# Kernel optimization log

Hardware: AMD Instinct MI355X
Metric: run time of the kernel (lower is better)

Reference implementation:

```python
import jax, jax.numpy as jnp
import numpy as np

SUB = 40   # subframe_size
NSUB = 4   # nb_subframes


def _glu(x, w):
    return x * jax.nn.sigmoid(x @ w.T)


def _gru(x, h, w_ih, w_hh):
    # torch.nn.GRUCell (bias=False): gates ordered r, z, n
    H = h.shape[-1]
    gi = x @ w_ih.T
    gh = h @ w_hh.T
    r = jax.nn.sigmoid(gi[:, :H] + gh[:, :H])
    z = jax.nn.sigmoid(gi[:, H:2 * H] + gh[:, H:2 * H])
    n = jnp.tanh(gi[:, 2 * H:] + r * gh[:, 2 * H:])
    return (1.0 - z) * n + z * h


def _fargan_forward(features, period, p):
    B, T, _ = features.shape
    period = jnp.clip(period, 32, 254)

    # ---- FARGANCond ----
    f = features[:, 2:, :]                               # [B, T-2, 20]
    pidx = jnp.clip(period[:, 2:] - 32, 0, 223)
    pe = p['pembed'][pidx]                               # [B, T-2, 12]
    x = jnp.tanh(jnp.concatenate([f, pe], -1) @ p['fd1_w'].T)   # [B, T-2, 64]
    y = jax.lax.conv_general_dilated(
        x.transpose(0, 2, 1), p['fconv1_w'], (1,), 'VALID',
        dimension_numbers=('NCH', 'OIH', 'NCH'))
    y = jnp.tanh(y).transpose(0, 2, 1)                   # [B, T-4, 128]
    cond = jnp.tanh(y @ p['fd2_w'].T)                    # [B, T-4, 320]

    nb_frames = T - 4
    cond_steps = cond.reshape(B, nb_frames, NSUB, 80)
    cond_steps = cond_steps.transpose(1, 2, 0, 3).reshape(nb_frames * NSUB, B, 80)
    pitch = period[:, 3:3 + nb_frames]                   # conv-center aligned pitch
    pitch_steps = jnp.repeat(pitch.T, NSUB, axis=0)      # [steps, B]

    rng = jnp.arange(SUB + 4)

    def step(carry, inp):
        exc_mem, prev_pred, s1, s2, s3, fwc_state = carry
        cond80, per = inp
        gain = 0.2 + 0.8 * jax.nn.sigmoid(cond80 @ p['cg_w'].T + p['cg_b'])
        gain = jnp.clip(gain, 0.001, 20.0)               # [B, 1]
        idx = 256 - per[:, None] + rng[None, :] - 2
        idx = idx - (idx >= 256) * per[:, None]
        idx = jnp.clip(idx, 0, 255)
        pred = jnp.take_along_axis(exc_mem, idx, axis=1) / (1e-5 + gain)  # [B, 44]
        prev = exc_mem[:, -SUB:] / (1e-5 + gain)         # [B, 40]
        tmp = jnp.concatenate([cond80, pred, prev], 1)   # [B, 164]
        fpitch = pred[:, 2:-2]                           # [B, 40]
        xcat = jnp.concatenate([fwc_state, tmp], 1)      # [B, 328]
        fwc_out = _glu(jnp.tanh(xcat @ p['fwc_w'].T), p['fwc_glu_w'])  # [B, 192]
        new_fwc_state = xcat[:, 164:]
        pg = jax.nn.sigmoid(fwc_out @ p['gout_w'].T + p['gout_b'])     # [B, 4]
        s1n = _gru(jnp.concatenate([fwc_out, pg[:, 0:1] * fpitch, prev], 1), s1, p['g1_ih'], p['g1_hh'])
        g1 = _glu(s1n, p['glu1_w'])
        s2n = _gru(jnp.concatenate([g1, pg[:, 1:2] * fpitch, prev], 1), s2, p['g2_ih'], p['g2_hh'])
        g2 = _glu(s2n, p['glu2_w'])
        s3n = _gru(jnp.concatenate([g2, pg[:, 2:3] * fpitch, prev], 1), s3, p['g3_ih'], p['g3_hh'])
        g3 = _glu(s3n, p['glu3_w'])
        skip_in = jnp.concatenate([g1, g2, g3, fwc_out, pg[:, 3:4] * fpitch, prev], 1)  # [B, 688+80]
        skip = _glu(jnp.tanh(skip_in @ p['skip_w'].T), p['skip_glu_w'])
        sig = jnp.tanh(skip @ p['sig_w'].T) * gain       # [B, 40]
        exc_mem = jnp.concatenate([exc_mem[:, SUB:], sig], 1)
        prev_pred = jnp.concatenate([prev_pred[:, SUB:], fpitch], 1)
        return (exc_mem, prev_pred, s1n, s2n, s3n, new_fwc_state), sig

    dt = features.dtype
    carry0 = (jnp.zeros((B, 256), dt), jnp.zeros((B, 256), dt),
              jnp.zeros((B, 160), dt), jnp.zeros((B, 128), dt),
              jnp.zeros((B, 128), dt), jnp.zeros((B, 164), dt))
    _, sigs = jax.lax.scan(jax.checkpoint(step), carry0, (cond_steps, pitch_steps))
    return sigs.transpose(1, 0, 2).reshape(B, -1)        # [B, nb_frames*160]


def _w(key, out_dim, in_dim):
    return jax.random.normal(key, (out_dim, in_dim), jnp.float32) / np.sqrt(in_dim)


def setup_inputs() -> dict:
    key = jax.random.key(0)
    ks = jax.random.split(key, 24)
    B, T = 128, 504
    d = {}
    d['features'] = jax.random.normal(ks[0], (B, T, 20), jnp.float32)
    d['period'] = jax.random.randint(ks[1], (B, T), 32, 255)
    d['pembed'] = jax.random.normal(ks[2], (224, 12), jnp.float32) * 0.3
    d['fd1_w'] = _w(ks[3], 64, 32)
    d['fconv1_w'] = jax.random.normal(ks[4], (128, 64, 3), jnp.float32) / np.sqrt(192.0)
    d['fd2_w'] = _w(ks[5], 320, 128)
    d['cg_w'] = _w(ks[6], 1, 80)
    d['cg_b'] = jnp.zeros((1,), jnp.float32)
    d['fwc_w'] = _w(ks[7], 192, 328)
    d['fwc_glu_w'] = _w(ks[8], 192, 192)
    d['g1_ih'] = _w(ks[9], 480, 272)
    d['g1_hh'] = _w(ks[10], 480, 160)
    d['glu1_w'] = _w(ks[11], 160, 160)
    d['g2_ih'] = _w(ks[12], 384, 240)
    d['g2_hh'] = _w(ks[13], 384, 128)
    d['glu2_w'] = _w(ks[14], 128, 128)
    d['g3_ih'] = _w(ks[15], 384, 208)
    d['g3_hh'] = _w(ks[16], 384, 128)
    d['glu3_w'] = _w(ks[17], 128, 128)
    d['skip_w'] = _w(ks[18], 128, 688)
    d['skip_glu_w'] = _w(ks[19], 128, 128)
    d['sig_w'] = _w(ks[20], 40, 128)
    d['gout_w'] = _w(ks[21], 4, 192)
    d['gout_b'] = jnp.zeros((4,), jnp.float32)
    return d


def reference(features, period, pembed, fd1_w, fconv1_w, fd2_w, cg_w, cg_b,
              fwc_w, fwc_glu_w, g1_ih, g1_hh, glu1_w, g2_ih, g2_hh, glu2_w,
              g3_ih, g3_hh, glu3_w, skip_w, skip_glu_w, sig_w, gout_w, gout_b):
    p = dict(pembed=pembed, fd1_w=fd1_w, fconv1_w=fconv1_w, fd2_w=fd2_w,
             cg_w=cg_w, cg_b=cg_b, fwc_w=fwc_w, fwc_glu_w=fwc_glu_w,
             g1_ih=g1_ih, g1_hh=g1_hh, glu1_w=glu1_w,
             g2_ih=g2_ih, g2_hh=g2_hh, glu2_w=glu2_w,
             g3_ih=g3_ih, g3_hh=g3_hh, glu3_w=glu3_w,
             skip_w=skip_w, skip_glu_w=skip_glu_w, sig_w=sig_w,
             gout_w=gout_w, gout_b=gout_b)
    return _fargan_forward(features, period, p)
```

## Files before the change

kernel.cpp:

```cpp
#include <hip/hip_runtime.h>
#include <hip/hip_fp16.h>
#include <math.h>


#define DEV __device__ __forceinline__

DEV float sigm(float x) { return 1.0f / (1.0f + __expf(-x)); }
DEV float tanh_f(float x) { return 1.0f - 2.0f / (__expf(2.0f * x) + 1.0f); }

typedef _Float16 h2v __attribute__((ext_vector_type(2)));

#if defined(__has_builtin)
#if __has_builtin(__builtin_amdgcn_fdot2)
#define HAVE_FDOT2 1
#endif
#endif

DEV float fdot2(h2v a, h2v b, float c) {
#ifdef HAVE_FDOT2
    return __builtin_amdgcn_fdot2(a, b, c, false);
#else
    return c + (float)a[0] * (float)b[0] + (float)a[1] * (float)b[1];
#endif
}

constexpr size_t STEPS = 2000;
constexpr size_t OFF_X     = 0;
constexpr size_t OFF_Y     = 4200000;
constexpr size_t OFF_GAIN  = 12392000;
constexpr size_t OFF_CONDH = 12648000;
constexpr size_t OFF_W     = 22888000;

constexpr size_t W_FWC     = 0;
constexpr size_t W_FWCGLU  = W_FWC    + 192*352;
constexpr size_t W_GOUT    = W_FWCGLU + 192*192;
constexpr size_t W_G1IH    = W_GOUT   + 4*192;
constexpr size_t W_G1HH    = W_G1IH   + 480*272;
constexpr size_t W_GLU1    = W_G1HH   + 480*160;
constexpr size_t W_G2IH    = W_GLU1   + 160*160;
constexpr size_t W_G2HH    = W_G2IH   + 384*240;
constexpr size_t W_GLU2    = W_G2HH   + 384*128;
constexpr size_t W_G3IH    = W_GLU2   + 128*128;
constexpr size_t W_G3HH    = W_G3IH   + 384*208;
constexpr size_t W_GLU3    = W_G3HH   + 384*128;
constexpr size_t W_SKIP    = W_GLU3   + 128*128;
constexpr size_t W_SKIPGLU = W_SKIP   + 128*704;
constexpr size_t W_SIG     = W_SKIPGLU+ 128*128;

__global__ void k_pack_h(const float* __restrict__ src, __half* __restrict__ dst,
                         int OUT, int K, int KP8) {
    int t = blockIdx.x * 256 + threadIdx.x;
    if (t >= OUT * KP8) return;
    int j = t % OUT;
    int k8 = t / OUT;
    __half* d = dst + (size_t)t * 8;
#pragma unroll
    for (int i = 0; i < 8; ++i) {
        int k = k8 * 8 + i;
        d[i] = (k < K) ? __float2half(src[(size_t)j * K + k]) : __float2half(0.0f);
    }
}

__global__ void k_feat(const float* __restrict__ features, const int* __restrict__ period,
                       const float* __restrict__ pembed, const float* __restrict__ fd1,
                       float* __restrict__ xbuf) {
    int t = blockIdx.x * 256 + threadIdx.x;
    const int total = 128 * 502 * 64;
    if (t >= total) return;
    int o = t & 63;
    int r = t >> 6;
    int ft = r % 502;
    int b = r / 502;
    const float* f = features + ((size_t)b * 504 + ft + 2) * 20;
    int per = period[b * 504 + ft + 2];
    per = min(max(per, 32), 254);
    const float* pe = pembed + (per - 32) * 12;
    const float* w = fd1 + o * 32;
    float acc = 0.0f;
#pragma unroll
    for (int i = 0; i < 20; ++i) acc += f[i] * w[i];
#pragma unroll
    for (int i = 0; i < 12; ++i) acc += pe[i] * w[20 + i];
    xbuf[t] = tanh_f(acc);
}

__global__ void k_conv(const float* __restrict__ xbuf, const float* __restrict__ fconv1,
                       float* __restrict__ ybuf) {
    int t = blockIdx.x * 256 + threadIdx.x;
    const int total = 128 * 500 * 128;
    if (t >= total) return;
    int oc = t & 127;
    int r = t >> 7;
    int tt = r % 500;
    int b = r / 500;
    const float* xp = xbuf + ((size_t)b * 502 + tt) * 64;
    const float* w = fconv1 + oc * 192;
    float acc = 0.0f;
#pragma unroll 8
    for (int i = 0; i < 64; ++i) {
        acc += xp[i] * w[i * 3 + 0];
        acc += xp[64 + i] * w[i * 3 + 1];
        acc += xp[128 + i] * w[i * 3 + 2];
    }
    ybuf[t] = tanh_f(acc);
}

__global__ void k_cond(const float* __restrict__ ybuf, const float* __restrict__ fd2,
                       __half* __restrict__ cond) {
    int b = blockIdx.x / 50;
    int t0 = (blockIdx.x % 50) * 10;
    int tid = threadIdx.x;
    __shared__ float yl[1280];
    for (int i = tid; i < 1280; i += 320)
        yl[i] = ybuf[((size_t)b * 500 + t0) * 128 + i];
    __syncthreads();
    const float* w = fd2 + tid * 128;
    float acc[10];
#pragma unroll
    for (int q = 0; q < 10; ++q) acc[q] = 0.0f;
#pragma unroll 4
    for (int k = 0; k < 128; ++k) {
        float wv = w[k];
#pragma unroll
        for (int q = 0; q < 10; ++q) acc[q] += wv * yl[q * 128 + k];
    }
#pragma unroll
    for (int q = 0; q < 10; ++q)
        cond[((size_t)b * 500 + t0 + q) * 320 + tid] = __float2half(tanh_f(acc[q]));
}

__global__ void k_gain(const __half* __restrict__ cond, const float* __restrict__ cgw,
                       const float* __restrict__ cgb, float* __restrict__ gains) {
    int t = blockIdx.x * 256 + threadIdx.x;
    const int total = 128 * 2000;
    if (t >= total) return;
    int s = t % 2000;
    int b = t / 2000;
    int frame = s >> 2, sub = s & 3;
    const __half* c = cond + ((size_t)b * 500 + frame) * 320 + sub * 80;
    float acc = 0.0f;
#pragma unroll 8
    for (int i = 0; i < 80; ++i) acc += __half2float(c[i]) * cgw[i];
    float g = 0.2f + 0.8f * sigm(acc + cgb[0]);
    g = fminf(20.0f, fmaxf(0.001f, g));
    gains[t] = g;
}

DEV void dot8h(uint4 w, uint4 x, float& a0, float& a1) {
    const h2v* wv = (const h2v*)&w;
    const h2v* xv = (const h2v*)&x;
    a0 = fdot2(wv[0], xv[0], a0);
    a1 = fdot2(wv[1], xv[1], a1);
    a0 = fdot2(wv[2], xv[2], a0);
    a1 = fdot2(wv[3], xv[3], a1);
}

template <int OUT, int KP8, int S>
DEV void mv_partial(const uint4* __restrict__ WT, const __half* __restrict__ x,
                    float* __restrict__ part, int tid) {
    static_assert(KP8 % S == 0, "KP8 % S");
    static_assert(OUT * S <= 1024, "threads");
    constexpr int KS8 = KP8 / S;
    if (tid < OUT * S) {
        int j = tid % OUT;
        int sl = tid / OUT;
        const uint4* w = WT + (size_t)sl * KS8 * OUT + j;
        const uint4* xx = (const uint4*)x + (size_t)sl * KS8;
        float a0 = 0.0f, a1 = 0.0f;
#pragma unroll 4
        for (int k = 0; k < KS8; ++k) {
            dot8h(w[(size_t)k * OUT], xx[k], a0, a1);
        }
        part[tid] = a0 + a1;
    }
}

template <int OUT, int KP8A, int KP8B>
DEV void gru_partial(const uint4* __restrict__ wa, const __half* __restrict__ xa,
                     const uint4* __restrict__ wb, const __half* __restrict__ xb,
                     float* __restrict__ pa, float* __restrict__ pb, int tid) {
    static_assert((KP8A % 2 == 0) && (KP8B % 2 == 0), "even");
    constexpr int KA = KP8A / 2, KB = KP8B / 2;
    if (tid < OUT * 2) {
        int j = tid % OUT;
        int sl = tid / OUT;
        {
            const uint4* w = wa + (size_t)sl * KA * OUT + j;
            const uint4* xx = (const uint4*)xa + (size_t)sl * KA;
            float a0 = 0.0f, a1 = 0.0f;
#pragma unroll 4
            for (int k = 0; k < KA; ++k) dot8h(w[(size_t)k * OUT], xx[k], a0, a1);
            pa[tid] = a0 + a1;
        }
        {
            const uint4* w = wb + (size_t)sl * KB * OUT + j;
            const uint4* xx = (const uint4*)xb + (size_t)sl * KB;
            float b0 = 0.0f, b1 = 0.0f;
#pragma unroll 4
            for (int k = 0; k < KB; ++k) dot8h(w[(size_t)k * OUT], xx[k], b0, b1);
            pb[tid] = b0 + b1;
        }
    }
}

template <int H>
DEV void gru_update(const float* __restrict__ pa, const float* __restrict__ pb,
                    float* __restrict__ s, __half* __restrict__ sh, int tid) {
    constexpr int OUT = 3 * H;
    if (tid < H) {
        float gi_r = pa[tid] + pa[OUT + tid];
        float gh_r = pb[tid] + pb[OUT + tid];
        float gi_z = pa[H + tid] + pa[OUT + H + tid];
        float gh_z = pb[H + tid] + pb[OUT + H + tid];
        float gi_n = pa[2 * H + tid] + pa[OUT + 2 * H + tid];
        float gh_n = pb[2 * H + tid] + pb[OUT + 2 * H + tid];
        float r = sigm(gi_r + gh_r);
        float z = sigm(gi_z + gh_z);
        float n = tanh_f(gi_n + r * gh_n);
        float v = (1.0f - z) * n + z * s[tid];
        s[tid] = v;
        sh[tid] = __float2half(v);
    }
}

__global__ __launch_bounds__(1024) void fargan_main(const float* __restrict__ ws,
                                                    const int* __restrict__ period,
                                                    const float* __restrict__ goutb,
                                                    float* __restrict__ out) {
    const int b = blockIdx.x;
    const int tid = threadIdx.x;

    const __half* cond = (const __half*)(ws + OFF_CONDH);
    const float* gains = ws + OFF_GAIN;
    const __half* whb  = (const __half*)(ws + OFF_W);
    const uint4* wFWC     = (const uint4*)(whb + W_FWC);
    const uint4* wFWCGLU  = (const uint4*)(whb + W_FWCGLU);
    const uint4* wGOUT    = (const uint4*)(whb + W_GOUT);
    const uint4* wG1IH    = (const uint4*)(whb + W_G1IH);
    const uint4* wG1HH    = (const uint4*)(whb + W_G1HH);
    const uint4* wGLU1    = (const uint4*)(whb + W_GLU1);
    const uint4* wG2IH    = (const uint4*)(whb + W_G2IH);
    const uint4* wG2HH    = (const uint4*)(whb + W_G2HH);
    const uint4* wGLU2    = (const uint4*)(whb + W_GLU2);
    const uint4* wG3IH    = (const uint4*)(whb + W_G3IH);
    const uint4* wG3HH    = (const uint4*)(whb + W_G3HH);
    const uint4* wGLU3    = (const uint4*)(whb + W_GLU3);
    const uint4* wSKIP    = (const uint4*)(whb + W_SKIP);
    const uint4* wSKIPGLU = (const uint4*)(whb + W_SKIPGLU);
    const uint4* wSIG     = (const uint4*)(whb + W_SIG);

    __shared__ __align__(16) __half xcat_h[352];
    __shared__ __align__(16) __half inb_h[272];
    __shared__ __align__(16) __half fwcpre_h[192], fwcout_h[192];
    __shared__ __align__(16) __half s1_h[160], s2_h[128], s3_h[128];
    __shared__ __align__(16) __half g1_h[160], g2_h[128], g3_h[128];
    __shared__ __align__(16) __half skipin_h[704], skippre_h[128], skipout_h[128];
    __shared__ __align__(16) float exc[256];
    __shared__ __align__(16) float s1[160], s2[128], s3[128];
    __shared__ __align__(16) float partA[1024], partB[1024];
    __shared__ __align__(16) float fwcpre[192];
    __shared__ __align__(16) float pg[4];
    __shared__ __align__(16) float skippre[128];
    __shared__ __align__(16) float sigraw[40];

    for (int i = tid; i < 256; i += 1024) exc[i] = 0.0f;
    if (tid < 160) { s1[tid] = 0.0f; s1_h[tid] = __float2half(0.0f); }
    if (tid < 128) { s2[tid] = 0.0f; s3[tid] = 0.0f;
                     s2_h[tid] = __float2half(0.0f); s3_h[tid] = __float2half(0.0f); }
    if (tid < 164) xcat_h[tid] = __float2half(0.0f);
    if (tid >= 328 && tid < 352) xcat_h[tid] = __float2half(0.0f);
    if (tid >= 688 && tid < 704) skipin_h[tid] = __float2half(0.0f);
    __syncthreads();

    for (int s = 0; s < (int)STEPS; ++s) {
        const int frame = s >> 2;
        const float gain = gains[(size_t)b * 2000 + s];
        const float ig = 1.0f / (1e-5f + gain);
        int per = period[b * 504 + 3 + frame];
        per = min(max(per, 32), 254);

        if (tid < 80) {
            xcat_h[164 + tid] = cond[((size_t)b * 500 + frame) * 320 + (s & 3) * 80 + tid];
        } else if (tid >= 128 && tid < 172) {
            int j = tid - 128;
            int idx = 254 - per + j;
            if (idx >= 256) idx -= per;
            idx = min(255, max(0, idx));
            xcat_h[244 + j] = __float2half(exc[idx] * ig);
        } else if (tid >= 192 && tid < 232) {
            xcat_h[288 + tid - 192] = __float2half(exc[216 + tid - 192] * ig);
        }
        __syncthreads();

        mv_partial<192, 44, 4>(wFWC, xcat_h, partA, tid);
        __syncthreads();
        if (tid < 192) {
            float a = partA[tid] + partA[192 + tid] + partA[384 + tid] + partA[576 + tid];
            float t = tanh_f(a);
            fwcpre[tid] = t;
            fwcpre_h[tid] = __float2half(t);
        }
        __syncthreads();

        mv_partial<192, 24, 4>(wFWCGLU, fwcpre_h, partA, tid);
        if (tid >= 768 && tid < 800) {
            int t2 = tid - 768;
            int j = t2 & 3, sl = t2 >> 2;
            const uint4* w = wGOUT + (sl * 3) * 4 + j;
            const uint4* xx = (const uint4*)fwcpre_h + sl * 3;
            float a0 = 0.0f, a1 = 0.0f;
#pragma unroll
            for (int k = 0; k < 3; ++k) dot8h(w[k * 4], xx[k], a0, a1);
            partB[t2] = a0 + a1;
        } else if (tid >= 832 && tid < 996) {
            xcat_h[tid - 832] = xcat_h[tid - 832 + 164];
        }
        __syncthreads();

        if (tid < 192) {
            float a = partA[tid] + partA[192 + tid] + partA[384 + tid] + partA[576 + tid];
            float v = fwcpre[tid] * sigm(a);
            __half vh = __float2half(v);
            fwcout_h[tid] = vh;
            inb_h[tid] = vh;
        } else if (tid < 232) {
            float a = goutb[0];
#pragma unroll
            for (int sl = 0; sl < 8; ++sl) a += partB[sl * 4];
            inb_h[tid] = __float2half(sigm(a) * __half2float(xcat_h[246 + tid - 192]));
        } else if (tid < 272) {
            inb_h[tid] = xcat_h[288 + tid - 232];
        } else if (tid >= 960 && tid < 964) {
            int j = tid - 960;
            float a = goutb[j];
#pragma unroll
            for (int sl = 0; sl < 8; ++sl) a += partB[sl * 4 + j];
            pg[j] = sigm(a);
        }
        __syncthreads();

        gru_partial<480, 34, 20>(wG1IH, inb_h, wG1HH, s1_h, partA, partB, tid);
        __syncthreads();
        gru_update<160>(partA, partB, s1, s1_h, tid);
        __syncthreads();

        mv_partial<160, 20, 4>(wGLU1, s1_h, partA, tid);
        __syncthreads();
        if (tid < 160) {
            float a = partA[tid] + partA[160 + tid] + partA[320 + tid] + partA[480 + tid];
            float v = s1[tid] * sigm(a);
            __half vh = __float2half(v);
            g1_h[tid] = vh;
            inb_h[tid] = vh;
        } else if (tid < 200) {
            inb_h[tid] = __float2half(pg[1] * __half2float(xcat_h[246 + tid - 160]));
        } else if (tid < 240) {
            inb_h[tid] = xcat_h[288 + tid - 200];
        }
        __syncthreads();

        gru_partial<384, 30, 16>(wG2IH, inb_h, wG2HH, s2_h, partA, partB, tid);
        __syncthreads();
        gru_update<128>(partA, partB, s2, s2_h, tid);
        __syncthreads();

        mv_partial<128, 16, 8>(wGLU2, s2_h, partA, tid);
        __syncthreads();
        if (tid < 128) {
            float a = 0.0f;
#pragma unroll
            for (int sl = 0; sl < 8; ++sl) a += partA[sl * 128 + tid];
            float v = s2[tid] * sigm(a);
            __half vh = __float2half(v);
            g2_h[tid] = vh;
            inb_h[tid] = vh;
        } else if (tid < 168) {
            inb_h[tid] = __float2half(pg[2] * __half2float(xcat_h[246 + tid - 128]));
        } else if (tid < 208) {
            inb_h[tid] = xcat_h[288 + tid - 168];
        }
        __syncthreads();

        gru_partial<384, 26, 16>(wG3IH, inb_h, wG3HH, s3_h, partA, partB, tid);
        __syncthreads();
        gru_update<128>(partA, partB, s3, s3_h, tid);
        __syncthreads();

        mv_partial<128, 16, 8>(wGLU3, s3_h, partA, tid);
        __syncthreads();
        if (tid < 128) {
            float a = 0.0f;
#pragma unroll
            for (int sl = 0; sl < 8; ++sl) a += partA[sl * 128 + tid];
            float v = s3[tid] * sigm(a);
            __half vh = __float2half(v);
            g3_h[tid] = vh;
            skipin_h[288 + tid] = vh;
        } else if (tid < 288) {
            skipin_h[tid - 128] = g1_h[tid - 128];
        } else if (tid < 416) {
            skipin_h[160 + tid - 288] = g2_h[tid - 288];
        } else if (tid < 608) {
            skipin_h[tid] = fwcout_h[tid - 416];
        } else if (tid < 648) {
            skipin_h[tid] = __float2half(pg[3] * __half2float(xcat_h[246 + tid - 608]));
        } else if (tid < 688) {
            skipin_h[tid] = xcat_h[288 + tid - 648];
        }
        __syncthreads();

        mv_partial<128, 88, 8>(wSKIP, skipin_h, partA, tid);
        __syncthreads();
        if (tid < 128) {
            float a = 0.0f;
#pragma unroll
            for (int sl = 0; sl < 8; ++sl) a += partA[sl * 128 + tid];
            float t = tanh_f(a);
            skippre[tid] = t;
            skippre_h[tid] = __float2half(t);
        }
        __syncthreads();

        mv_partial<128, 16, 8>(wSKIPGLU, skippre_h, partA, tid);
        __syncthreads();
        if (tid < 128) {
            float a = 0.0f;
#pragma unroll
            for (int sl = 0; sl < 8; ++sl) a += partA[sl * 128 + tid];
            skipout_h[tid] = __float2half(skippre[tid] * sigm(a));
        }
        __syncthreads();

        mv_partial<40, 16, 8>(wSIG, skipout_h, partA, tid);
        __syncthreads();
        float keep = (tid < 216) ? exc[tid + 40] : 0.0f;
        if (tid < 40) {
            float a = 0.0f;
#pragma unroll
            for (int sl = 0; sl < 8; ++sl) a += partA[sl * 40 + tid];
            sigraw[tid] = tanh_f(a) * gain;
        }
        __syncthreads();
        if (tid < 216) {
            exc[tid] = keep;
        } else if (tid < 256) {
            float sv = sigraw[tid - 216];
            exc[tid] = sv;
            out[(size_t)b * 80000 + (size_t)s * 40 + (tid - 216)] = sv;
        }
        __syncthreads();
    }
}

extern "C" void kernel_launch(void* const* d_in, const int* in_sizes, int n_in,
                              void* d_out, int out_size, void* d_ws, size_t ws_size,
                              hipStream_t stream) {
    const float* features = (const float*)d_in[0];
    const int*   period   = (const int*)d_in[1];
    const float* pembed   = (const float*)d_in[2];
    const float* fd1_w    = (const float*)d_in[3];
    const float* fconv1_w = (const float*)d_in[4];
    const float* fd2_w    = (const float*)d_in[5];
    const float* cg_w     = (const float*)d_in[6];
    const float* cg_b     = (const float*)d_in[7];
    const float* fwc_w    = (const float*)d_in[8];
    const float* fwc_glu  = (const float*)d_in[9];
    const float* g1_ih    = (const float*)d_in[10];
    const float* g1_hh    = (const float*)d_in[11];
    const float* glu1_w   = (const float*)d_in[12];
    const float* g2_ih    = (const float*)d_in[13];
    const float* g2_hh    = (const float*)d_in[14];
    const float* glu2_w   = (const float*)d_in[15];
    const float* g3_ih    = (const float*)d_in[16];
    const float* g3_hh    = (const float*)d_in[17];
    const float* glu3_w   = (const float*)d_in[18];
    const float* skip_w   = (const float*)d_in[19];
    const float* skip_glu = (const float*)d_in[20];
    const float* sig_w    = (const float*)d_in[21];
    const float* gout_w   = (const float*)d_in[22];
    const float* gout_b   = (const float*)d_in[23];

    float* ws = (float*)d_ws;
    float* out = (float*)d_out;
    __half* wh = (__half*)(ws + OFF_W);

    struct PW { const float* src; size_t off; int out, k, kpad; };
    const PW pws[15] = {
        {fwc_w,    W_FWC,     192, 328, 352}, {fwc_glu, W_FWCGLU, 192, 192, 192},
        {gout_w,   W_GOUT,      4, 192, 192}, {g1_ih,   W_G1IH,   480, 272, 272},
        {g1_hh,    W_G1HH,    480, 160, 160}, {glu1_w,  W_GLU1,   160, 160, 160},
        {g2_ih,    W_G2IH,    384, 240, 240}, {g2_hh,   W_G2HH,   384, 128, 128},
        {glu2_w,   W_GLU2,    128, 128, 128}, {g3_ih,   W_G3IH,   384, 208, 208},
        {g3_hh,    W_G3HH,    384, 128, 128}, {glu3_w,  W_GLU3,   128, 128, 128},
        {skip_w,   W_SKIP,    128, 688, 704}, {skip_glu,W_SKIPGLU,128, 128, 128},
        {sig_w,    W_SIG,      40, 128, 128},
    };
    for (int i = 0; i < 15; ++i) {
        int kp8 = pws[i].kpad / 8;
        int n = pws[i].out * kp8;
        k_pack_h<<<(n + 255) / 256, 256, 0, stream>>>(pws[i].src, wh + pws[i].off,
                                                      pws[i].out, pws[i].k, kp8);
    }

    {
        int n = 128 * 502 * 64;
        k_feat<<<(n + 255) / 256, 256, 0, stream>>>(features, period, pembed, fd1_w,
                                                    ws + OFF_X);
    }
    {
        int n = 128 * 500 * 128;
        k_conv<<<(n + 255) / 256, 256, 0, stream>>>(ws + OFF_X, fconv1_w, ws + OFF_Y);
    }
    k_cond<<<128 * 50, 320, 0, stream>>>(ws + OFF_Y, fd2_w, (__half*)(ws + OFF_CONDH));
    {
        int n = 128 * 2000;
        k_gain<<<(n + 255) / 256, 256, 0, stream>>>((const __half*)(ws + OFF_CONDH),
                                                    cg_w, cg_b, ws + OFF_GAIN);
    }

    fargan_main<<<128, 1024, 0, stream>>>(ws, period, gout_b, out);
}
```

Baseline: 36.20 ms.

## Interleave weight layout for wave-shuffle reductions, cache GLU weights in LDS, use ring buffer

Repacks the non-GRU matrices so the K-slices for each output sit next to each other within a wavefront. The partial sums are then reduced with shuffle-xor instead of a shared-memory partial array, which drops one barrier per matvec. It also caches the fwc_glu, glu2 and glu3 weights in LDS (about 139KB), replaces the excitation shift with a circular ring buffer, and writes skip inputs in place. The intent is to cut barriers and global weight traffic in the sequential recurrent loop, at the cost of heavy LDS use and more complex indexing.

```diff
diff --git a/kernel.cpp b/kernel.cpp
--- a/kernel.cpp
+++ b/kernel.cpp
@@ -31,21 +31,26 @@
 constexpr size_t OFF_CONDH = 12648000;
 constexpr size_t OFF_W     = 22888000;
 
-constexpr size_t W_FWC     = 0;
-constexpr size_t W_FWCGLU  = W_FWC    + 192*352;
-constexpr size_t W_GOUT    = W_FWCGLU + 192*192;
-constexpr size_t W_G1IH    = W_GOUT   + 4*192;
-constexpr size_t W_G1HH    = W_G1IH   + 480*272;
-constexpr size_t W_GLU1    = W_G1HH   + 480*160;
-constexpr size_t W_G2IH    = W_GLU1   + 160*160;
-constexpr size_t W_G2HH    = W_G2IH   + 384*240;
-constexpr size_t W_GLU2    = W_G2HH   + 384*128;
-constexpr size_t W_G3IH    = W_GLU2   + 128*128;
-constexpr size_t W_G3HH    = W_G3IH   + 384*208;
-constexpr size_t W_GLU3    = W_G3HH   + 384*128;
-constexpr size_t W_SKIP    = W_GLU3   + 128*128;
-constexpr size_t W_SKIPGLU = W_SKIP   + 128*704;
-constexpr size_t W_SIG     = W_SKIPGLU+ 128*128;
+constexpr size_t W_GOUT  = 0;
+constexpr size_t W_G1IH  = 768;
+constexpr size_t W_G1HH  = W_G1IH + 480*272;
+constexpr size_t W_G2IH  = W_G1HH + 480*160;
+constexpr size_t W_G2HH  = W_G2IH + 384*240;
+constexpr size_t W_G3IH  = W_G2HH + 384*128;
+constexpr size_t W_G3HH  = W_G3IH + 384*208;
+constexpr size_t I_FWC     = W_G3HH + 384*128;
+constexpr size_t I_FWCGLU  = I_FWC + 192*352;
+constexpr size_t I_GLU1    = I_FWCGLU + 192*192;
+constexpr size_t I_GLU2    = I_GLU1 + 160*160;
+constexpr size_t I_GLU3    = I_GLU2 + 128*128;
+constexpr size_t I_SKIP    = I_GLU3 + 128*128;
+constexpr size_t I_SKIPGLU = I_SKIP + 128*704;
+constexpr size_t I_SIG     = I_SKIPGLU + 128*128;
+
+constexpr int WL_FWCGLU = 0;
+constexpr int WL_GLU2   = 4608;
+constexpr int WL_GLU3   = 6656;
+constexpr int WL_TOT    = 8704;
 
 __global__ void k_pack_h(const float* __restrict__ src, __half* __restrict__ dst,
                          int OUT, int K, int KP8) {
@@ -58,6 +63,24 @@
     for (int i = 0; i < 8; ++i) {
         int k = k8 * 8 + i;
         d[i] = (k < K) ? __float2half(src[(size_t)j * K + k]) : __float2half(0.0f);
+    }
+}
+
+__global__ void k_pack_i(const float* __restrict__ src, __half* __restrict__ dst,
+                         int OUT, int K, int KP8, int LS) {
+    int t = blockIdx.x * 256 + threadIdx.x;
+    if (t >= OUT * KP8) return;
+    int KS8 = KP8 / LS;
+    int k = t / (OUT * LS);
+    int rem = t % (OUT * LS);
+    int j = rem / LS;
+    int sl = rem % LS;
+    int k8 = sl * KS8 + k;
+    __half* d = dst + (size_t)t * 8;
+#pragma unroll
+    for (int i = 0; i < 8; ++i) {
+        int kk = k8 * 8 + i;
+        d[i] = (kk < K) ? __float2half(src[(size_t)j * K + kk]) : __float2half(0.0f);
     }
 }
 
@@ -155,31 +178,38 @@
     a1 = fdot2(wv[3], xv[3], a1);
 }
 
-template <int OUT, int KP8, int S>
-DEV void mv_partial(const uint4* __restrict__ WT, const __half* __restrict__ x,
-                    float* __restrict__ part, int tid) {
-    static_assert(KP8 % S == 0, "KP8 % S");
-    static_assert(OUT * S <= 1024, "threads");
-    constexpr int KS8 = KP8 / S;
-    if (tid < OUT * S) {
-        int j = tid % OUT;
-        int sl = tid / OUT;
-        const uint4* w = WT + (size_t)sl * KS8 * OUT + j;
-        const uint4* xx = (const uint4*)x + (size_t)sl * KS8;
-        float a0 = 0.0f, a1 = 0.0f;
-#pragma unroll 4
-        for (int k = 0; k < KS8; ++k) {
-            dot8h(w[(size_t)k * OUT], xx[k], a0, a1);
-        }
-        part[tid] = a0 + a1;
-    }
+template <int OUT, int KS8, int LS>
+DEV float mv_red_i(const uint4* __restrict__ W, const __half* __restrict__ x, int tid) {
+    const int sl = tid % LS;
+    const uint4* w = W + tid;
+    const uint4* xx = (const uint4*)x + sl * KS8;
+    float a0 = 0.0f, a1 = 0.0f;
+#pragma unroll
+    for (int k = 0; k < KS8; ++k) dot8h(w[(size_t)k * (OUT * LS)], xx[k], a0, a1);
+    float a = a0 + a1;
+#pragma unroll
+    for (int m = 1; m < LS; m <<= 1) a += __shfl_xor(a, m, 64);
+    return a;
+}
+
+template <int OUT, int KS8, int LS>
+DEV float mv_red_l(const uint4* wl, const __half* __restrict__ x, int tid) {
+    const int sl = tid % LS;
+    const uint4* w = wl + tid;
+    const uint4* xx = (const uint4*)x + sl * KS8;
+    float a0 = 0.0f, a1 = 0.0f;
+#pragma unroll
+    for (int k = 0; k < KS8; ++k) dot8h(w[(size_t)k * (OUT * LS)], xx[k], a0, a1);
+    float a = a0 + a1;
+#pragma unroll
+    for (int m = 1; m < LS; m <<= 1) a += __shfl_xor(a, m, 64);
+    return a;
 }
 
 template <int OUT, int KP8A, int KP8B>
 DEV void gru_partial(const uint4* __restrict__ wa, const __half* __restrict__ xa,
                      const uint4* __restrict__ wb, const __half* __restrict__ xb,
                      float* __restrict__ pa, float* __restrict__ pb, int tid) {
-    static_assert((KP8A % 2 == 0) && (KP8B % 2 == 0), "even");
     constexpr int KA = KP8A / 2, KB = KP8B / 2;
     if (tid < OUT * 2) {
         int j = tid % OUT;
@@ -233,37 +263,42 @@
     const __half* cond = (const __half*)(ws + OFF_CONDH);
     const float* gains = ws + OFF_GAIN;
     const __half* whb  = (const __half*)(ws + OFF_W);
-    const uint4* wFWC     = (const uint4*)(whb + W_FWC);
-    const uint4* wFWCGLU  = (const uint4*)(whb + W_FWCGLU);
-    const uint4* wGOUT    = (const uint4*)(whb + W_GOUT);
-    const uint4* wG1IH    = (const uint4*)(whb + W_G1IH);
-    const uint4* wG1HH    = (const uint4*)(whb + W_G1HH);
-    const uint4* wGLU1    = (const uint4*)(whb + W_GLU1);
-    const uint4* wG2IH    = (const uint4*)(whb + W_G2IH);
-    const uint4* wG2HH    = (const uint4*)(whb + W_G2HH);
-    const uint4* wGLU2    = (const uint4*)(whb + W_GLU2);
-    const uint4* wG3IH    = (const uint4*)(whb + W_G3IH);
-    const uint4* wG3HH    = (const uint4*)(whb + W_G3HH);
-    const uint4* wGLU3    = (const uint4*)(whb + W_GLU3);
-    const uint4* wSKIP    = (const uint4*)(whb + W_SKIP);
-    const uint4* wSKIPGLU = (const uint4*)(whb + W_SKIPGLU);
-    const uint4* wSIG     = (const uint4*)(whb + W_SIG);
+    const uint4* wGOUT   = (const uint4*)(whb + W_GOUT);
+    const uint4* wG1IH   = (const uint4*)(whb + W_G1IH);
+    const uint4* wG1HH   = (const uint4*)(whb + W_G1HH);
+    const uint4* wG2IH   = (const uint4*)(whb + W_G2IH);
+    const uint4* wG2HH   = (const uint4*)(whb + W_G2HH);
+    const uint4* wG3IH   = (const uint4*)(whb + W_G3IH);
+    const uint4* wG3HH   = (const uint4*)(whb + W_G3HH);
+    const uint4* iFWC     = (const uint4*)(whb + I_FWC);
+    const uint4* iFWCGLU  = (const uint4*)(whb + I_FWCGLU);
+    const uint4* iGLU1    = (const uint4*)(whb + I_GLU1);
+    const uint4* iGLU2    = (const uint4*)(whb + I_GLU2);
+    const uint4* iGLU3    = (const uint4*)(whb + I_GLU3);
+    const uint4* iSKIP    = (const uint4*)(whb + I_SKIP);
+    const uint4* iSKIPGLU = (const uint4*)(whb + I_SKIPGLU);
+    const uint4* iSIG     = (const uint4*)(whb + I_SIG);
+
+    __shared__ __align__(16) uint4 wlds[WL_TOT];
 
     __shared__ __align__(16) __half xcat_h[352];
     __shared__ __align__(16) __half inb_h[272];
     __shared__ __align__(16) __half fwcpre_h[192], fwcout_h[192];
     __shared__ __align__(16) __half s1_h[160], s2_h[128], s3_h[128];
-    __shared__ __align__(16) __half g1_h[160], g2_h[128], g3_h[128];
     __shared__ __align__(16) __half skipin_h[704], skippre_h[128], skipout_h[128];
-    __shared__ __align__(16) float exc[256];
+    __shared__ __align__(16) float ring[256];
     __shared__ __align__(16) float s1[160], s2[128], s3[128];
     __shared__ __align__(16) float partA[1024], partB[1024];
-    __shared__ __align__(16) float fwcpre[192];
+    __shared__ __align__(16) float fwcpre[192], skippre[128];
     __shared__ __align__(16) float pg[4];
-    __shared__ __align__(16) float skippre[128];
-    __shared__ __align__(16) float sigraw[40];
-
-    for (int i = tid; i < 256; i += 1024) exc[i] = 0.0f;
+
+    for (int i = tid; i < 4608; i += 1024) wlds[WL_FWCGLU + i] = iFWCGLU[i];
+    for (int i = tid; i < 2048; i += 1024) {
+        wlds[WL_GLU2 + i] = iGLU2[i];
+        wlds[WL_GLU3 + i] = iGLU3[i];
+    }
+
+    for (int i = tid; i < 256; i += 1024) ring[i] = 0.0f;
     if (tid < 160) { s1[tid] = 0.0f; s1_h[tid] = __float2half(0.0f); }
     if (tid < 128) { s2[tid] = 0.0f; s3[tid] = 0.0f;
                      s2_h[tid] = __float2half(0.0f); s3_h[tid] = __float2half(0.0f); }
@@ -274,6 +309,7 @@
 
     for (int s = 0; s < (int)STEPS; ++s) {
         const int frame = s >> 2;
+        const int head = (s * 40) & 255;
         const float gain = gains[(size_t)b * 2000 + s];
         const float ig = 1.0f / (1e-5f + gain);
         int per = period[b * 504 + 3 + frame];
@@ -286,24 +322,36 @@
             int idx = 254 - per + j;
             if (idx >= 256) idx -= per;
             idx = min(255, max(0, idx));
-            xcat_h[244 + j] = __float2half(exc[idx] * ig);
+            xcat_h[244 + j] = __float2half(ring[(head + idx) & 255] * ig);
         } else if (tid >= 192 && tid < 232) {
-            xcat_h[288 + tid - 192] = __float2half(exc[216 + tid - 192] * ig);
-        }
-        __syncthreads();
-
-        mv_partial<192, 44, 4>(wFWC, xcat_h, partA, tid);
-        __syncthreads();
-        if (tid < 192) {
-            float a = partA[tid] + partA[192 + tid] + partA[384 + tid] + partA[576 + tid];
-            float t = tanh_f(a);
-            fwcpre[tid] = t;
-            fwcpre_h[tid] = __float2half(t);
-        }
-        __syncthreads();
-
-        mv_partial<192, 24, 4>(wFWCGLU, fwcpre_h, partA, tid);
-        if (tid >= 768 && tid < 800) {
+            int j = tid - 192;
+            __half vh = __float2half(ring[(head + 216 + j) & 255] * ig);
+            xcat_h[288 + j] = vh;
+            skipin_h[648 + j] = vh;
+        }
+        __syncthreads();
+
+        if (tid < 768) {
+            float a = mv_red_i<192, 11, 4>(iFWC, xcat_h, tid);
+            if ((tid & 3) == 0) {
+                int j = tid >> 2;
+                float t = tanh_f(a);
+                fwcpre[j] = t;
+                fwcpre_h[j] = __float2half(t);
+            }
+        }
+        __syncthreads();
+
+        if (tid < 768) {
+            float a = mv_red_l<192, 6, 4>(wlds + WL_FWCGLU, fwcpre_h, tid);
+            if ((tid & 3) == 0) {
+                int j = tid >> 2;
+                float v = fwcpre[j] * sigm(a);
+                __half vh = __float2half(v);
+                fwcout_h[j] = vh;
+                skipin_h[416 + j] = vh;
+            }
+        } else if (tid < 800) {
             int t2 = tid - 768;
             int j = t2 & 3, sl = t2 >> 2;
             const uint4* w = wGOUT + (sl * 3) * 4 + j;
@@ -318,11 +366,7 @@
         __syncthreads();
 
         if (tid < 192) {
-            float a = partA[tid] + partA[192 + tid] + partA[384 + tid] + partA[576 + tid];
-            float v = fwcpre[tid] * sigm(a);
-            __half vh = __float2half(v);
-            fwcout_h[tid] = vh;
-            inb_h[tid] = vh;
+            inb_h[tid] = fwcout_h[tid];
         } else if (tid < 232) {
             float a = goutb[0];
 #pragma unroll
@@ -330,6 +374,12 @@
             inb_h[tid] = __float2half(sigm(a) * __half2float(xcat_h[246 + tid - 192]));
         } else if (tid < 272) {
             inb_h[tid] = xcat_h[288 + tid - 232];
+        } else if (tid >= 288 && tid < 328) {
+            float a = goutb[3];
+#pragma unroll
+            for (int sl = 0; sl < 8; ++sl) a += partB[sl * 4 + 3];
+            skipin_h[608 + tid - 288] =
+                __float2half(sigm(a) * __half2float(xcat_h[246 + tid - 288]));
         } else if (tid >= 960 && tid < 964) {
             int j = tid - 960;
             float a = goutb[j];
@@ -342,42 +392,46 @@
         gru_partial<480, 34, 20>(wG1IH, inb_h, wG1HH, s1_h, partA, partB, tid);
         __syncthreads();
         gru_update<160>(partA, partB, s1, s1_h, tid);
-        __syncthreads();
-
-        mv_partial<160, 20, 4>(wGLU1, s1_h, partA, tid);
-        __syncthreads();
-        if (tid < 160) {
-            float a = partA[tid] + partA[160 + tid] + partA[320 + tid] + partA[480 + tid];
-            float v = s1[tid] * sigm(a);
-            __half vh = __float2half(v);
-            g1_h[tid] = vh;
-            inb_h[tid] = vh;
-        } else if (tid < 200) {
-            inb_h[tid] = __float2half(pg[1] * __half2float(xcat_h[246 + tid - 160]));
-        } else if (tid < 240) {
-            inb_h[tid] = xcat_h[288 + tid - 200];
+        if (tid >= 192 && tid < 232) {
+            inb_h[160 + tid - 192] =
+                __float2half(pg[1] * __half2float(xcat_h[246 + tid - 192]));
+        } else if (tid >= 232 && tid < 272) {
+            inb_h[200 + tid - 232] = xcat_h[288 + tid - 232];
+        }
+        __syncthreads();
+
+        if (tid < 640) {
+            float a = mv_red_i<160, 5, 4>(iGLU1, s1_h, tid);
+            if ((tid & 3) == 0) {
+                int j = tid >> 2;
+                float v = s1[j] * sigm(a);
+                __half vh = __float2half(v);
+                skipin_h[j] = vh;
+                inb_h[j] = vh;
+            }
         }
         __syncthreads();
 
         gru_partial<384, 30, 16>(wG2IH, inb_h, wG2HH, s2_h, partA, partB, tid);
         __syncthreads();
         gru_update<128>(partA, partB, s2, s2_h, tid);
-        __syncthreads();
-
-        mv_partial<128, 16, 8>(wGLU2, s2_h, partA, tid);
-        __syncthreads();
-        if (tid < 128) {
-            float a = 0.0f;
-#pragma unroll
-            for (int sl = 0; sl < 8; ++sl) a += partA[sl * 128 + tid];
-            float v = s2[tid] * sigm(a);
-            __half vh = __float2half(v);
-            g2_h[tid] = vh;
-            inb_h[tid] = vh;
-        } else if (tid < 168) {
-            inb_h[tid] = __float2half(pg[2] * __half2float(xcat_h[246 + tid - 128]));
-        } else if (tid < 208) {
-            inb_h[tid] = xcat_h[288 + tid - 168];
+        if (tid >= 160 && tid < 200) {
+            inb_h[128 + tid - 160] =
+                __float2half(pg[2] * __half2float(xcat_h[246 + tid - 160]));
+        } else if (tid >= 200 && tid < 240) {
+            inb_h[168 + tid - 200] = xcat_h[288 + tid - 200];
+        }
+        __syncthreads();
+
+        {
+            float a = mv_red_l<128, 2, 8>(wlds + WL_GLU2, s2_h, tid);
+            if ((tid & 7) == 0) {
+                int j = tid >> 3;
+                float v = s2[j] * sigm(a);
+                __half vh = __float2half(v);
+                skipin_h[160 + j] = vh;
+                inb_h[j] = vh;
+            }
         }
         __syncthreads();
 
@@ -386,67 +440,43 @@
         gru_update<128>(partA, partB, s3, s3_h, tid);
         __syncthreads();
 
-        mv_partial<128, 16, 8>(wGLU3, s3_h, partA, tid);
-        __syncthreads();
-        if (tid < 128) {
-            float a = 0.0f;
-#pragma unroll
-            for (int sl = 0; sl < 8; ++sl) a += partA[sl * 128 + tid];
-            float v = s3[tid] * sigm(a);
-            __half vh = __float2half(v);
-            g3_h[tid] = vh;
-            skipin_h[288 + tid] = vh;
-        } else if (tid < 288) {
-            skipin_h[tid - 128] = g1_h[tid - 128];
-        } else if (tid < 416) {
-            skipin_h[160 + tid - 288] = g2_h[tid - 288];
-        } else if (tid < 608) {
-            skipin_h[tid] = fwcout_h[tid - 416];
-        } else if (tid < 648) {
-            skipin_h[tid] = __float2half(pg[3] * __half2float(xcat_h[246 + tid - 608]));
-        } else if (tid < 688) {
-            skipin_h[tid] = xcat_h[288 + tid - 648];
-        }
-        __syncthreads();
-
-        mv_partial<128, 88, 8>(wSKIP, skipin_h, partA, tid);
-        __syncthreads();
-        if (tid < 128) {
-            float a = 0.0f;
-#pragma unroll
-            for (int sl = 0; sl < 8; ++sl) a += partA[sl * 128 + tid];
-            float t = tanh_f(a);
-            skippre[tid] = t;
-            skippre_h[tid] = __float2half(t);
-        }
-        __syncthreads();
-
-        mv_partial<128, 16, 8>(wSKIPGLU, skippre_h, partA, tid);
-        __syncthreads();
-        if (tid < 128) {
-            float a = 0.0f;
-#pragma unroll
-            for (int sl = 0; sl < 8; ++sl) a += partA[sl * 128 + tid];
-            skipout_h[tid] = __float2half(skippre[tid] * sigm(a));
-        }
-        __syncthreads();
-
-        mv_partial<40, 16, 8>(wSIG, skipout_h, partA, tid);
-        __syncthreads();
-        float keep = (tid < 216) ? exc[tid + 40] : 0.0f;
-        if (tid < 40) {
-            float a = 0.0f;
-#pragma unroll
-            for (int sl = 0; sl < 8; ++sl) a += partA[sl * 40 + tid];
-            sigraw[tid] = tanh_f(a) * gain;
-        }
-        __syncthreads();
-        if (tid < 216) {
-            exc[tid] = keep;
-        } else if (tid < 256) {
-            float sv = sigraw[tid - 216];
-            exc[tid] = sv;
-            out[(size_t)b * 80000 + (size_t)s * 40 + (tid - 216)] = sv;
+        {
+            float a = mv_red_l<128, 2, 8>(wlds + WL_GLU3, s3_h, tid);
+            if ((tid & 7) == 0) {
+                int j = tid >> 3;
+                skipin_h[288 + j] = __float2half(s3[j] * sigm(a));
+            }
+        }
+        __syncthreads();
+
+        {
+            float a = mv_red_i<128, 11, 8>(iSKIP, skipin_h, tid);
+            if ((tid & 7) == 0) {
+                int j = tid >> 3;
+                float t = tanh_f(a);
+                skippre[j] = t;
+                skippre_h[j] = __float2half(t);
+            }
+        }
+        __syncthreads();
+
+        {
+            float a = mv_red_i<128, 2, 8>(iSKIPGLU, skippre_h, tid);
+            if ((tid & 7) == 0) {
+                int j = tid >> 3;
+                skipout_h[j] = __float2half(skippre[j] * sigm(a));
+            }
+        }
+        __syncthreads();
+
+        if (tid < 320) {
+            float a = mv_red_i<40, 2, 8>(iSIG, skipout_h, tid);
+            if ((tid & 7) == 0) {
+                int j = tid >> 3;
+                float sv = tanh_f(a) * gain;
+                ring[(head + j) & 255] = sv;
+                out[(size_t)b * 80000 + (size_t)s * 40 + j] = sv;
+            }
         }
         __syncthreads();
     }
@@ -484,22 +514,33 @@
     float* out = (float*)d_out;
     __half* wh = (__half*)(ws + OFF_W);
 
-    struct PW { const float* src; size_t off; int out, k, kpad; };
-    const PW pws[15] = {
-        {fwc_w,    W_FWC,     192, 328, 352}, {fwc_glu, W_FWCGLU, 192, 192, 192},
-        {gout_w,   W_GOUT,      4, 192, 192}, {g1_ih,   W_G1IH,   480, 272, 272},
-        {g1_hh,    W_G1HH,    480, 160, 160}, {glu1_w,  W_GLU1,   160, 160, 160},
-        {g2_ih,    W_G2IH,    384, 240, 240}, {g2_hh,   W_G2HH,   384, 128, 128},
-        {glu2_w,   W_GLU2,    128, 128, 128}, {g3_ih,   W_G3IH,   384, 208, 208},
-        {g3_hh,    W_G3HH,    384, 128, 128}, {glu3_w,  W_GLU3,   128, 128, 128},
-        {skip_w,   W_SKIP,    128, 688, 704}, {skip_glu,W_SKIPGLU,128, 128, 128},
-        {sig_w,    W_SIG,      40, 128, 128},
+    struct PW { const float* src; size_t off; int out, k; };
+    const PW pws[7] = {
+        {gout_w, W_GOUT,   4, 192}, {g1_ih, W_G1IH, 480, 272},
+        {g1_hh,  W_G1HH, 480, 160}, {g2_ih, W_G2IH, 384, 240},
+        {g2_hh,  W_G2HH, 384, 128}, {g3_ih, W_G3IH, 384, 208},
+        {g3_hh,  W_G3HH, 384, 128},
     };
-    for (int i = 0; i < 15; ++i) {
-        int kp8 = pws[i].kpad / 8;
+    for (int i = 0; i < 7; ++i) {
+        int kp8 = pws[i].k / 8;
         int n = pws[i].out * kp8;
         k_pack_h<<<(n + 255) / 256, 256, 0, stream>>>(pws[i].src, wh + pws[i].off,
                                                       pws[i].out, pws[i].k, kp8);
+    }
+
+    struct PI { const float* src; size_t off; int out, k, kpad, ls; };
+    const PI pis[8] = {
+        {fwc_w,    I_FWC,     192, 328, 352, 4}, {fwc_glu, I_FWCGLU, 192, 192, 192, 4},
+        {glu1_w,   I_GLU1,    160, 160, 160, 4}, {glu2_w,  I_GLU2,   128, 128, 128, 8},
+        {glu3_w,   I_GLU3,    128, 128, 128, 8}, {skip_w,  I_SKIP,   128, 688, 704, 8},
+        {skip_glu, I_SKIPGLU, 128, 128, 128, 8}, {sig_w,   I_SIG,     40, 128, 128, 8},
+    };
+    for (int i = 0; i < 8; ++i) {
+        int kp8 = pis[i].kpad / 8;
+        int n = pis[i].out * kp8;
+        k_pack_i<<<(n + 255) / 256, 256, 0, stream>>>(pis[i].src, wh + pis[i].off,
+                                                      pis[i].out, pis[i].k, kp8,
+                                                      pis[i].ls);
     }
 
     {
```

Result: slower. 49.12 ms (+35.7%).
